# Kernel tuning notes

Measured on AMD Instinct MI355X. Metric: run time of the kernel, lower is better.

The kernel has to match this reference:

```python
import jax, jax.numpy as jnp
import numpy as np

N = 100000      # nodes
E = 1600000     # edges
F_IN = 256      # num_features
H = 128         # hidden_dim
C = 16          # num_classes
LOG_SIGMA0 = float(np.log(0.1))  # prior_sigma = 0.1


def setup_inputs() -> dict:
    key = jax.random.key(0)
    ks = jax.random.split(key, 8)
    x = jax.random.normal(ks[0], (N, F_IN), jnp.float32)
    edge_index = jax.random.randint(ks[1], (2, E), 0, N, dtype=jnp.int64)
    # GCNConv linear weight + bias
    W = jax.random.normal(ks[2], (F_IN, H), jnp.float32) / np.float32(np.sqrt(F_IN))
    gcn_b = jnp.zeros((H,), jnp.float32)
    # BayesLinear params (mu + log_sigma) and fixed sampled noise eps
    w_mu = jax.random.normal(ks[3], (C, H), jnp.float32) / np.float32(np.sqrt(H))
    w_log_sigma = jnp.full((C, H), LOG_SIGMA0, jnp.float32)
    b_mu = jnp.zeros((C,), jnp.float32)
    b_log_sigma = jnp.full((C,), LOG_SIGMA0, jnp.float32)
    eps_w = jax.random.normal(ks[4], (C, H), jnp.float32)
    eps_b = jax.random.normal(ks[5], (C,), jnp.float32)
    return {"x": x, "edge_index": edge_index, "W": W, "gcn_b": gcn_b,
            "w_mu": w_mu, "w_log_sigma": w_log_sigma,
            "b_mu": b_mu, "b_log_sigma": b_log_sigma,
            "eps_w": eps_w, "eps_b": eps_b}


def reference(x, edge_index, W, gcn_b, w_mu, w_log_sigma, b_mu, b_log_sigma, eps_w, eps_b):
    n = x.shape[0]
    # --- GCNConv: add self-loops, symmetric deg^{-1/2} normalization ---
    loop = jnp.arange(n, dtype=edge_index.dtype)
    src = jnp.concatenate([edge_index[0], loop])  # message source j
    dst = jnp.concatenate([edge_index[1], loop])  # aggregation target i
    deg = jax.ops.segment_sum(jnp.ones_like(dst, dtype=x.dtype), dst, num_segments=n)
    deg_inv_sqrt = jnp.where(deg > 0, jax.lax.rsqrt(deg), 0.0)
    norm = deg_inv_sqrt[src] * deg_inv_sqrt[dst]            # [E+N]
    h = x @ W                                               # [N,H] transform first
    msg = h[src] * norm[:, None]                            # [E+N,H] gather
    agg = jax.ops.segment_sum(msg, dst, num_segments=n)     # [N,H] scatter-add
    agg = agg + gcn_b
    # --- ReLU; dropout is identity in eval mode ---
    a = jax.nn.relu(agg)
    # --- BayesLinear: w = mu + exp(log_sigma) * eps ---
    w = w_mu + jnp.exp(w_log_sigma) * eps_w                 # [C,H]
    b = b_mu + jnp.exp(b_log_sigma) * eps_b                 # [C]
    logits = a @ w.T + b                                    # [N,C]
    return jax.nn.log_softmax(logits, axis=1)
```

## Files before the change

kernel.cpp:

```cpp
#include <hip/hip_runtime.h>
#include <hip/hip_bf16.h>

#define N_NODES 100000
#define F_IN    256
#define H_DIM   128
#define C_CLS   16
#define NB_SCAN ((N_NODES + 255) / 256)
#define NSHARD  8
#define SHARD_W ((N_NODES + NSHARD - 1) / NSHARD)
#define ZB      98

typedef __attribute__((ext_vector_type(8))) short  short8;
typedef __attribute__((ext_vector_type(4))) float  float4v;
typedef __attribute__((ext_vector_type(4))) unsigned short ushort4v;

__device__ __forceinline__ float b2f(ushort u) {
    union { unsigned int i; float f; } v;
    v.i = ((unsigned int)u) << 16;
    return v.f;
}

__device__ __forceinline__ ushort f2b(float f) {
    unsigned int x = __float_as_uint(f);
    unsigned int r = (x + 0x7FFFu + ((x >> 16) & 1u)) >> 16;
    return (ushort)r;
}

__device__ __forceinline__ float ldsel(const void* p, int i, int f32f) {
    return f32f ? ((const float*)p)[i] : b2f(((const ushort*)p)[i]);
}

__global__ __launch_bounds__(64) void sniff(const ushort* __restrict__ x,
                                            const int* __restrict__ ei,
                                            int* __restrict__ flags) {
    int lane = threadIdx.x;
    int cnt_bf = 0;
#pragma unroll
    for (int j = 0; j < 4; ++j) {
        ushort u = x[lane * 4 + j];
        int e = (u >> 7) & 0xFF;
        if ((e >= 100 && e <= 140) || (u & 0x7FFF) == 0) cnt_bf++;
    }
    int zodd = (ei[2 * lane + 1] == 0) ? 1 : 0;
#pragma unroll
    for (int off = 32; off >= 1; off >>= 1) {
        cnt_bf += __shfl_xor(cnt_bf, off, 64);
        zodd   += __shfl_xor(zodd,   off, 64);
    }
    if (lane == 0) {
        flags[0] = (cnt_bf < 230) ? 1 : 0;
        flags[1] = (zodd  >= 32) ? 1 : 0;
    }
}

__global__ __launch_bounds__(256) void prep_params(const int* __restrict__ flags,
                                                   const void* __restrict__ W_any,
                                                   ushort* __restrict__ wtg,
                                                   const void* __restrict__ w_mu,
                                                   const void* __restrict__ w_ls,
                                                   const void* __restrict__ eps_w,
                                                   const void* __restrict__ b_mu,
                                                   const void* __restrict__ b_ls,
                                                   const void* __restrict__ eps_b,
                                                   const void* __restrict__ gcn_b,
                                                   ushort* __restrict__ whi,
                                                   ushort* __restrict__ wlo,
                                                   float* __restrict__ bias16,
                                                   float* __restrict__ gcnb_f,
                                                   int* __restrict__ cnt) {
    const int f32f = flags[0];
    const int t = threadIdx.x;
    if (blockIdx.x < H_DIM) {
        const int n = blockIdx.x;
        float v = f32f ? ((const float*)W_any)[t * H_DIM + n]
                       : b2f(((const ushort*)W_any)[t * H_DIM + n]);
        wtg[n * F_IN + t] = f2b(v);
        return;
    }
    if (blockIdx.x > H_DIM) {
        int idx4 = (blockIdx.x - H_DIM - 1) * 256 + t;
        if (idx4 < N_NODES / 4) ((int4*)cnt)[idx4] = make_int4(0, 0, 0, 0);
        return;
    }
#pragma unroll
    for (int i = t; i < C_CLS * H_DIM; i += 256) {
        float v = ldsel(w_mu, i, f32f) + __expf(ldsel(w_ls, i, f32f)) * ldsel(eps_w, i, f32f);
        ushort h = f2b(v);
        whi[i] = h;
        wlo[i] = f2b(v - b2f(h));
    }
    if (t < C_CLS)
        bias16[t] = ldsel(b_mu, t, f32f) + __expf(ldsel(b_ls, t, f32f)) * ldsel(eps_b, t, f32f);
    if (t < H_DIM)
        gcnb_f[t] = ldsel(gcn_b, t, f32f);
}

__global__ __launch_bounds__(256) void prep(const int* __restrict__ flags,
                                            const int* __restrict__ ei,
                                            int* __restrict__ cnt,
                                            int2* __restrict__ pr,
                                            int* __restrict__ rk, int E) {
    int e = blockIdx.x * 256 + threadIdx.x;
    if (e >= E) return;
    int i64 = flags[1];
    int s = i64 ? ei[2L * e]          : ei[e];
    int d = i64 ? ei[2L * E + 2L * e] : ei[(long)E + e];
    pr[e] = make_int2(s, d);
    rk[e] = atomicAdd(&cnt[d], 1);
}

__global__ __launch_bounds__(256) void scan1(const int* __restrict__ cnt,
                                             int* __restrict__ offs,
                                             int* __restrict__ bsum) {
    __shared__ int sd[256];
    int t = threadIdx.x;
    int i = blockIdx.x * 256 + t;
    int v = (i < N_NODES) ? cnt[i] : 0;
    sd[t] = v;
    __syncthreads();
#pragma unroll
    for (int d = 1; d < 256; d <<= 1) {
        int add = (t >= d) ? sd[t - d] : 0;
        __syncthreads();
        sd[t] += add;
        __syncthreads();
    }
    if (i < N_NODES) offs[i] = sd[t] - v;
    if (t == 255) bsum[blockIdx.x] = sd[255];
}

__global__ __launch_bounds__(256) void scan23(int* __restrict__ offs,
                                              const int* __restrict__ bsum,
                                              const int* __restrict__ cnt,
                                              float* __restrict__ dis, int E) {
    __shared__ int ws[4];
    const int t = threadIdx.x;
    const int bid = blockIdx.x;
    const int lane = t & 63;
    const int wave = t >> 6;

    int acc = 0;
    for (int j = t; j < bid; j += 256) acc += bsum[j];
#pragma unroll
    for (int off = 32; off >= 1; off >>= 1) acc += __shfl_xor(acc, off, 64);
    if (lane == 0) ws[wave] = acc;
    __syncthreads();
    const int boffb = ws[0] + ws[1] + ws[2] + ws[3];

    int i = bid * 256 + t;
    if (i == 0) offs[N_NODES] = E;
    if (i >= N_NODES) return;
    offs[i] += boffb;
    dis[i] = rsqrtf((float)(cnt[i] + 1));
}

__global__ __launch_bounds__(256) void build_perm(const int2* __restrict__ pr,
                                                  const int* __restrict__ rk,
                                                  const int* __restrict__ offs,
                                                  int* __restrict__ perm, int E) {
    const int shard = blockIdx.x & (NSHARD - 1);
    const int jb    = blockIdx.x >> 3;
    const int nb    = gridDim.x >> 3;
    const int lo = shard * SHARD_W;
    const int hi = lo + SHARD_W;
    for (int e = jb * 256 + threadIdx.x; e < E; e += nb * 256) {
        int2 p = pr[e];
        if (p.y >= lo && p.y < hi)
            perm[offs[p.y] + rk[e]] = p.x;
    }
}

__global__ __launch_bounds__(256) void gemm_xw(const int* __restrict__ flags,
                                               const void* __restrict__ x_any,
                                               const ushort* __restrict__ wtg,
                                               const float* __restrict__ dis,
                                               ushort* __restrict__ hout) {
    __shared__ __align__(16) ushort wt[128 * 128];
    const int f32f = flags[0];

    const int tid  = threadIdx.x;
    const int lane = tid & 63;
    const int quad = lane >> 4;
    const int lm   = lane & 15;
    const int wave = tid >> 6;

    const int rbase = blockIdx.x * 128 + wave * 32;
    int arow0 = rbase + lm;
    int arow1 = rbase + 16 + lm;
    if (arow0 >= N_NODES) arow0 = N_NODES - 1;
    if (arow1 >= N_NODES) arow1 = N_NODES - 1;
    const float*  xrf0 = (const float*) x_any + (size_t)arow0 * F_IN;
    const float*  xrf1 = (const float*) x_any + (size_t)arow1 * F_IN;
    const ushort* xrb0 = (const ushort*)x_any + (size_t)arow0 * F_IN;
    const ushort* xrb1 = (const ushort*)x_any + (size_t)arow1 * F_IN;

    float4v acc0[8], acc1[8];
#pragma unroll
    for (int c = 0; c < 8; ++c) {
        acc0[c] = (float4v){0.f, 0.f, 0.f, 0.f};
        acc1[c] = (float4v){0.f, 0.f, 0.f, 0.f};
    }

    for (int hh = 0; hh < 2; ++hh) {
        if (hh) __syncthreads();
#pragma unroll
        for (int it = 0; it < 8; ++it) {
            int flat = (it * 256 + tid) * 8;
            int col  = flat >> 7;
            int kloc = flat & 127;
            short8 v = *(const short8*)(wtg + col * F_IN + hh * 128 + kloc);
            int dst = ((col << 7) | kloc) ^ ((col & 7) << 3);
            *(short8*)(wt + dst) = v;
        }
        __syncthreads();
#pragma unroll
        for (int s = 0; s < 4; ++s) {
            int klocal = s * 32 + quad * 8;
            short8 afrag0, afrag1;
            if (f32f) {
                const float* p0 = xrf0 + hh * 128 + klocal;
                const float* p1 = xrf1 + hh * 128 + klocal;
                float4 u0 = *(const float4*)p0;
                float4 u1 = *(const float4*)(p0 + 4);
                float4 u2 = *(const float4*)p1;
                float4 u3 = *(const float4*)(p1 + 4);
                afrag0[0] = (short)f2b(u0.x); afrag0[1] = (short)f2b(u0.y);
                afrag0[2] = (short)f2b(u0.z); afrag0[3] = (short)f2b(u0.w);
                afrag0[4] = (short)f2b(u1.x); afrag0[5] = (short)f2b(u1.y);
                afrag0[6] = (short)f2b(u1.z); afrag0[7] = (short)f2b(u1.w);
                afrag1[0] = (short)f2b(u2.x); afrag1[1] = (short)f2b(u2.y);
                afrag1[2] = (short)f2b(u2.z); afrag1[3] = (short)f2b(u2.w);
                afrag1[4] = (short)f2b(u3.x); afrag1[5] = (short)f2b(u3.y);
                afrag1[6] = (short)f2b(u3.z); afrag1[7] = (short)f2b(u3.w);
            } else {
                afrag0 = *(const short8*)(xrb0 + hh * 128 + klocal);
                afrag1 = *(const short8*)(xrb1 + hh * 128 + klocal);
            }
#pragma unroll
            for (int c = 0; c < 8; ++c) {
                int colr = c * 16 + lm;
                int src = ((colr << 7) | klocal) ^ ((lm & 7) << 3);
                short8 bfrag = *(const short8*)(wt + src);
                acc0[c] = __builtin_amdgcn_mfma_f32_16x16x32_bf16(afrag0, bfrag, acc0[c], 0, 0, 0);
                acc1[c] = __builtin_amdgcn_mfma_f32_16x16x32_bf16(afrag1, bfrag, acc1[c], 0, 0, 0);
            }
        }
    }
    float dv0[4], dv1[4];
#pragma unroll
    for (int r = 0; r < 4; ++r) {
        int n0 = rbase + quad * 4 + r;
        int n1 = rbase + 16 + quad * 4 + r;
        dv0[r] = (n0 < N_NODES) ? dis[n0] : 0.f;
        dv1[r] = (n1 < N_NODES) ? dis[n1] : 0.f;
    }
#pragma unroll
    for (int c = 0; c < 8; ++c) {
        int col = c * 16 + lm;
#pragma unroll
        for (int r = 0; r < 4; ++r) {
            int n0 = rbase + quad * 4 + r;
            int n1 = rbase + 16 + quad * 4 + r;
            if (n0 < N_NODES) hout[(size_t)n0 * H_DIM + col] = f2b(acc0[c][r] * dv0[r]);
            if (n1 < N_NODES) hout[(size_t)n1 * H_DIM + col] = f2b(acc1[c][r] * dv1[r]);
        }
    }
}

__global__ __launch_bounds__(256) void gather_final(const int* __restrict__ flags,
                                                    const int* __restrict__ offs,
                                                    const int* __restrict__ perm,
                                                    const float* __restrict__ dis,
                                                    const ushort* __restrict__ hb,
                                                    const float* __restrict__ gcnb_f,
                                                    const ushort* __restrict__ whi,
                                                    const ushort* __restrict__ wlo,
                                                    const float* __restrict__ bias16,
                                                    void* __restrict__ out) {
    __shared__ __align__(16) ushort alds[16][136];
    const int f32f = flags[0];
    const int lane = threadIdx.x & 63;
    const int wave = threadIdx.x >> 6;
    const int n0 = blockIdx.x * 16;

    for (int r = 0; r < 4; ++r) {
        const int node = n0 + wave * 4 + r;
        const int off0 = __builtin_amdgcn_readfirstlane(offs[node]);
        const int deg  = __builtin_amdgcn_readfirstlane(offs[node + 1]) - off0;
        const int* pp = perm + off0;

        float ax = 0.f, ay = 0.f;
        const int full = deg & ~15;
        for (int base = 0; base < full; base += 16) {
#pragma unroll
            for (int k = 0; k < 16; ++k) {
                int sk = pp[base + k];
                uint u = *((const uint*)(hb + (size_t)sk * H_DIM) + lane);
                ax += __uint_as_float(u << 16);
                ay += __uint_as_float(u & 0xFFFF0000u);
            }
        }
        {
            const int nb = deg - full;
#pragma unroll
            for (int k = 0; k < 16; ++k) {
                int   sk = 0;
                float wk = 0.f;
                if (k < nb) { sk = pp[full + k]; wk = 1.f; }
                uint u = *((const uint*)(hb + (size_t)sk * H_DIM) + lane);
                ax = fmaf(wk, __uint_as_float(u << 16),         ax);
                ay = fmaf(wk, __uint_as_float(u & 0xFFFF0000u), ay);
            }
        }

        const float dd = dis[node];
        uint us = *((const uint*)(hb + (size_t)node * H_DIM) + lane);
        float2 gb = *(const float2*)(gcnb_f + 2 * lane);
        ax = (ax + __uint_as_float(us << 16))         * dd + gb.x;
        ay = (ay + __uint_as_float(us & 0xFFFF0000u)) * dd + gb.y;
        ax = fmaxf(ax, 0.f);
        ay = fmaxf(ay, 0.f);
        uint pack = (uint)f2b(ax) | ((uint)f2b(ay) << 16);
        *((uint*)&alds[wave * 4 + r][2 * lane]) = pack;
    }
    __syncthreads();
    if (wave != 0) return;

    const int lm = lane & 15, quad = lane >> 4;
    const ushort* bh = whi + lm * H_DIM + quad * 8;
    const ushort* bl = wlo + lm * H_DIM + quad * 8;

    float4v acc = (float4v){0.f, 0.f, 0.f, 0.f};
#pragma unroll
    for (int s = 0; s < 4; ++s) {
        short8 af = *(const short8*)&alds[lm][quad * 8 + s * 32];
        short8 b0 = *(const short8*)(bh + s * 32);
        short8 b1 = *(const short8*)(bl + s * 32);
        acc = __builtin_amdgcn_mfma_f32_16x16x32_bf16(af, b0, acc, 0, 0, 0);
        acc = __builtin_amdgcn_mfma_f32_16x16x32_bf16(af, b1, acc, 0, 0, 0);
    }

    const float bias = bias16[lm];
    float p[4], m[4], ss[4];
#pragma unroll
    for (int r = 0; r < 4; ++r) { p[r] = acc[r] + bias; m[r] = p[r]; }
#pragma unroll
    for (int off = 1; off < 16; off <<= 1)
#pragma unroll
        for (int r = 0; r < 4; ++r) m[r] = fmaxf(m[r], __shfl_xor(m[r], off, 64));
#pragma unroll
    for (int r = 0; r < 4; ++r) ss[r] = __expf(p[r] - m[r]);
#pragma unroll
    for (int off = 1; off < 16; off <<= 1)
#pragma unroll
        for (int r = 0; r < 4; ++r) ss[r] += __shfl_xor(ss[r], off, 64);

    if (f32f) {
        float* op = (float*)out;
#pragma unroll
        for (int r = 0; r < 4; ++r)
            op[(size_t)(n0 + quad * 4 + r) * C_CLS + lm] = p[r] - m[r] - __logf(ss[r]);
    } else {
        ushort* op = (ushort*)out;
#pragma unroll
        for (int r = 0; r < 4; ++r)
            op[(size_t)(n0 + quad * 4 + r) * C_CLS + lm] = f2b(p[r] - m[r] - __logf(ss[r]));
    }
}

extern "C" void kernel_launch(void* const* d_in, const int* in_sizes, int n_in,
                              void* d_out, int out_size, void* d_ws, size_t ws_size,
                              hipStream_t stream) {
    const int E = in_sizes[1] / 2;

    char* wp = (char*)d_ws;
    auto alloc = [&](size_t bytes) -> char* {
        char* p = wp; wp += (bytes + 511) & ~(size_t)511; return p;
    };
    int*    flags  = (int*)   alloc(64);
    ushort* hb     = (ushort*)alloc((size_t)N_NODES * H_DIM * 2);
    int*    cnt    = (int*)   alloc((size_t)N_NODES * 4);
    int*    offs   = (int*)   alloc((size_t)(N_NODES + 1) * 4);
    int*    bsum   = (int*)   alloc((size_t)NB_SCAN * 4);
    float*  dis    = (float*) alloc((size_t)N_NODES * 4);
    int*    perm   = (int*)   alloc((size_t)E * 4);
    int2*   pr     = (int2*)  alloc((size_t)E * 8);
    int*    rk     = (int*)   alloc((size_t)E * 4);
    ushort* wtg    = (ushort*)alloc((size_t)H_DIM * F_IN * 2);
    ushort* whi    = (ushort*)alloc((size_t)C_CLS * H_DIM * 2);
    ushort* wlo    = (ushort*)alloc((size_t)C_CLS * H_DIM * 2);
    float*  bias16 = (float*) alloc((size_t)C_CLS * 4);
    float*  gcnb_f = (float*) alloc((size_t)H_DIM * 4);

    sniff<<<1, 64, 0, stream>>>((const ushort*)d_in[0], (const int*)d_in[1], flags);
    prep_params<<<H_DIM + 1 + ZB, 256, 0, stream>>>(flags, d_in[2], wtg,
                                  d_in[4], d_in[5], d_in[8],
                                  d_in[6], d_in[7], d_in[9], d_in[3],
                                  whi, wlo, bias16, gcnb_f, cnt);
    prep<<<(E + 255) / 256, 256, 0, stream>>>(flags, (const int*)d_in[1], cnt, pr, rk, E);
    scan1<<<NB_SCAN, 256, 0, stream>>>(cnt, offs, bsum);
    scan23<<<NB_SCAN, 256, 0, stream>>>(offs, bsum, cnt, dis, E);
    build_perm<<<2048, 256, 0, stream>>>(pr, rk, offs, perm, E);
    gemm_xw<<<(N_NODES + 127) / 128, 256, 0, stream>>>(flags, d_in[0], wtg, dis, hb);
    gather_final<<<N_NODES / 16, 256, 0, stream>>>(flags, offs, perm, dis, hb,
                                                   gcnb_f, whi, wlo, bias16, (void*)d_out);
}
```

Before: 376.2 us.

## Replace CSR build with fixed-width ELL adjacency plus overflow list

Drops the count/scan/permutation pipeline (prep, two scan kernels, build_perm) in favour of one sharded scatter kernel. It writes each edge's source straight into a fixed 64-slot per-node ELL row, with an atomic overflow list for nodes of higher degree. Degree normalisation is now computed inline from the counts, so the separate dis array goes away. This saves several launches and the intermediate pair/rank buffers. The cost is a larger padded ELL array (100k×64 ints) and a linear scan of the overflow list for high-degree nodes.

```diff
diff --git a/kernel.cpp b/kernel.cpp
--- a/kernel.cpp
+++ b/kernel.cpp
@@ -5,9 +5,9 @@
 #define F_IN    256
 #define H_DIM   128
 #define C_CLS   16
-#define NB_SCAN ((N_NODES + 255) / 256)
 #define NSHARD  8
 #define SHARD_W ((N_NODES + NSHARD - 1) / NSHARD)
+#define MAXDEG  64
 #define ZB      98
 
 typedef __attribute__((ext_vector_type(8))) short  short8;
@@ -67,7 +67,8 @@
                                                    ushort* __restrict__ wlo,
                                                    float* __restrict__ bias16,
                                                    float* __restrict__ gcnb_f,
-                                                   int* __restrict__ cnt) {
+                                                   int* __restrict__ cnt,
+                                                   int* __restrict__ ocnt) {
     const int f32f = flags[0];
     const int t = threadIdx.x;
     if (blockIdx.x < H_DIM) {
@@ -82,6 +83,7 @@
         if (idx4 < N_NODES / 4) ((int4*)cnt)[idx4] = make_int4(0, 0, 0, 0);
         return;
     }
+    if (t == 0) *ocnt = 0;
 #pragma unroll
     for (int i = t; i < C_CLS * H_DIM; i += 256) {
         float v = ldsel(w_mu, i, f32f) + __expf(ldsel(w_ls, i, f32f)) * ldsel(eps_w, i, f32f);
@@ -95,85 +97,33 @@
         gcnb_f[t] = ldsel(gcn_b, t, f32f);
 }
 
-__global__ __launch_bounds__(256) void prep(const int* __restrict__ flags,
-                                            const int* __restrict__ ei,
-                                            int* __restrict__ cnt,
-                                            int2* __restrict__ pr,
-                                            int* __restrict__ rk, int E) {
-    int e = blockIdx.x * 256 + threadIdx.x;
-    if (e >= E) return;
-    int i64 = flags[1];
-    int s = i64 ? ei[2L * e]          : ei[e];
-    int d = i64 ? ei[2L * E + 2L * e] : ei[(long)E + e];
-    pr[e] = make_int2(s, d);
-    rk[e] = atomicAdd(&cnt[d], 1);
-}
-
-__global__ __launch_bounds__(256) void scan1(const int* __restrict__ cnt,
-                                             int* __restrict__ offs,
-                                             int* __restrict__ bsum) {
-    __shared__ int sd[256];
-    int t = threadIdx.x;
-    int i = blockIdx.x * 256 + t;
-    int v = (i < N_NODES) ? cnt[i] : 0;
-    sd[t] = v;
-    __syncthreads();
-#pragma unroll
-    for (int d = 1; d < 256; d <<= 1) {
-        int add = (t >= d) ? sd[t - d] : 0;
-        __syncthreads();
-        sd[t] += add;
-        __syncthreads();
-    }
-    if (i < N_NODES) offs[i] = sd[t] - v;
-    if (t == 255) bsum[blockIdx.x] = sd[255];
-}
-
-__global__ __launch_bounds__(256) void scan23(int* __restrict__ offs,
-                                              const int* __restrict__ bsum,
-                                              const int* __restrict__ cnt,
-                                              float* __restrict__ dis, int E) {
-    __shared__ int ws[4];
-    const int t = threadIdx.x;
-    const int bid = blockIdx.x;
-    const int lane = t & 63;
-    const int wave = t >> 6;
-
-    int acc = 0;
-    for (int j = t; j < bid; j += 256) acc += bsum[j];
-#pragma unroll
-    for (int off = 32; off >= 1; off >>= 1) acc += __shfl_xor(acc, off, 64);
-    if (lane == 0) ws[wave] = acc;
-    __syncthreads();
-    const int boffb = ws[0] + ws[1] + ws[2] + ws[3];
-
-    int i = bid * 256 + t;
-    if (i == 0) offs[N_NODES] = E;
-    if (i >= N_NODES) return;
-    offs[i] += boffb;
-    dis[i] = rsqrtf((float)(cnt[i] + 1));
-}
-
-__global__ __launch_bounds__(256) void build_perm(const int2* __restrict__ pr,
-                                                  const int* __restrict__ rk,
-                                                  const int* __restrict__ offs,
-                                                  int* __restrict__ perm, int E) {
+__global__ __launch_bounds__(256) void ell_scatter(const int* __restrict__ flags,
+                                                   const int* __restrict__ ei,
+                                                   int* __restrict__ cnt,
+                                                   int* __restrict__ ell,
+                                                   int2* __restrict__ ovf,
+                                                   int* __restrict__ ocnt, int E) {
     const int shard = blockIdx.x & (NSHARD - 1);
     const int jb    = blockIdx.x >> 3;
     const int nb    = gridDim.x >> 3;
     const int lo = shard * SHARD_W;
     const int hi = lo + SHARD_W;
-    for (int e = jb * 256 + threadIdx.x; e < E; e += nb * 256) {
-        int2 p = pr[e];
-        if (p.y >= lo && p.y < hi)
-            perm[offs[p.y] + rk[e]] = p.x;
+    const int i64 = flags[1];
+    for (long e = (long)jb * 256 + threadIdx.x; e < E; e += (long)nb * 256) {
+        int d = i64 ? ei[2L * E + 2L * e] : ei[(long)E + e];
+        if (d >= lo && d < hi) {
+            int s = i64 ? ei[2L * e] : ei[e];
+            int rk = atomicAdd(&cnt[d], 1);
+            if (rk < MAXDEG) ell[(long)d * MAXDEG + rk] = s;
+            else { int oi = atomicAdd(ocnt, 1); ovf[oi] = make_int2(s, d); }
+        }
     }
 }
 
 __global__ __launch_bounds__(256) void gemm_xw(const int* __restrict__ flags,
                                                const void* __restrict__ x_any,
                                                const ushort* __restrict__ wtg,
-                                               const float* __restrict__ dis,
+                                               const int* __restrict__ cnt,
                                                ushort* __restrict__ hout) {
     __shared__ __align__(16) ushort wt[128 * 128];
     const int f32f = flags[0];
@@ -251,8 +201,8 @@
     for (int r = 0; r < 4; ++r) {
         int n0 = rbase + quad * 4 + r;
         int n1 = rbase + 16 + quad * 4 + r;
-        dv0[r] = (n0 < N_NODES) ? dis[n0] : 0.f;
-        dv1[r] = (n1 < N_NODES) ? dis[n1] : 0.f;
+        dv0[r] = (n0 < N_NODES) ? rsqrtf((float)(cnt[n0] + 1)) : 0.f;
+        dv1[r] = (n1 < N_NODES) ? rsqrtf((float)(cnt[n1] + 1)) : 0.f;
     }
 #pragma unroll
     for (int c = 0; c < 8; ++c) {
@@ -268,9 +218,10 @@
 }
 
 __global__ __launch_bounds__(256) void gather_final(const int* __restrict__ flags,
-                                                    const int* __restrict__ offs,
-                                                    const int* __restrict__ perm,
-                                                    const float* __restrict__ dis,
+                                                    const int* __restrict__ cnt,
+                                                    const int* __restrict__ ell,
+                                                    const int2* __restrict__ ovf,
+                                                    const int* __restrict__ ocnt,
                                                     const ushort* __restrict__ hb,
                                                     const float* __restrict__ gcnb_f,
                                                     const ushort* __restrict__ whi,
@@ -285,9 +236,9 @@
 
     for (int r = 0; r < 4; ++r) {
         const int node = n0 + wave * 4 + r;
-        const int off0 = __builtin_amdgcn_readfirstlane(offs[node]);
-        const int deg  = __builtin_amdgcn_readfirstlane(offs[node + 1]) - off0;
-        const int* pp = perm + off0;
+        const int degt = __builtin_amdgcn_readfirstlane(cnt[node]);
+        const int deg  = degt < MAXDEG ? degt : MAXDEG;
+        const int* pp = ell + (long)node * MAXDEG;
 
         float ax = 0.f, ay = 0.f;
         const int full = deg & ~15;
@@ -312,8 +263,19 @@
                 ay = fmaf(wk, __uint_as_float(u & 0xFFFF0000u), ay);
             }
         }
-
-        const float dd = dis[node];
+        if (degt > MAXDEG) {
+            const int no = __builtin_amdgcn_readfirstlane(*ocnt);
+            for (int j = 0; j < no; ++j) {
+                int2 o = ovf[j];
+                if (o.y == node) {
+                    uint u = *((const uint*)(hb + (size_t)o.x * H_DIM) + lane);
+                    ax += __uint_as_float(u << 16);
+                    ay += __uint_as_float(u & 0xFFFF0000u);
+                }
+            }
+        }
+
+        const float dd = rsqrtf((float)(degt + 1));
         uint us = *((const uint*)(hb + (size_t)node * H_DIM) + lane);
         float2 gb = *(const float2*)(gcnb_f + 2 * lane);
         ax = (ax + __uint_as_float(us << 16))         * dd + gb.x;
@@ -380,12 +342,9 @@
     int*    flags  = (int*)   alloc(64);
     ushort* hb     = (ushort*)alloc((size_t)N_NODES * H_DIM * 2);
     int*    cnt    = (int*)   alloc((size_t)N_NODES * 4);
-    int*    offs   = (int*)   alloc((size_t)(N_NODES + 1) * 4);
-    int*    bsum   = (int*)   alloc((size_t)NB_SCAN * 4);
-    float*  dis    = (float*) alloc((size_t)N_NODES * 4);
-    int*    perm   = (int*)   alloc((size_t)E * 4);
-    int2*   pr     = (int2*)  alloc((size_t)E * 8);
-    int*    rk     = (int*)   alloc((size_t)E * 4);
+    int*    ell    = (int*)   alloc((size_t)N_NODES * MAXDEG * 4);
+    int2*   ovf    = (int2*)  alloc((size_t)E * 8);
+    int*    ocnt   = (int*)   alloc(64);
     ushort* wtg    = (ushort*)alloc((size_t)H_DIM * F_IN * 2);
     ushort* whi    = (ushort*)alloc((size_t)C_CLS * H_DIM * 2);
     ushort* wlo    = (ushort*)alloc((size_t)C_CLS * H_DIM * 2);
@@ -396,12 +355,9 @@
     prep_params<<<H_DIM + 1 + ZB, 256, 0, stream>>>(flags, d_in[2], wtg,
                                   d_in[4], d_in[5], d_in[8],
                                   d_in[6], d_in[7], d_in[9], d_in[3],
-                                  whi, wlo, bias16, gcnb_f, cnt);
-    prep<<<(E + 255) / 256, 256, 0, stream>>>(flags, (const int*)d_in[1], cnt, pr, rk, E);
-    scan1<<<NB_SCAN, 256, 0, stream>>>(cnt, offs, bsum);
-    scan23<<<NB_SCAN, 256, 0, stream>>>(offs, bsum, cnt, dis, E);
-    build_perm<<<2048, 256, 0, stream>>>(pr, rk, offs, perm, E);
-    gemm_xw<<<(N_NODES + 127) / 128, 256, 0, stream>>>(flags, d_in[0], wtg, dis, hb);
-    gather_final<<<N_NODES / 16, 256, 0, stream>>>(flags, offs, perm, dis, hb,
+                                  whi, wlo, bias16, gcnb_f, cnt, ocnt);
+    ell_scatter<<<2048, 256, 0, stream>>>(flags, (const int*)d_in[1], cnt, ell, ovf, ocnt, E);
+    gemm_xw<<<(N_NODES + 127) / 128, 256, 0, stream>>>(flags, d_in[0], wtg, cnt, hb);
+    gather_final<<<N_NODES / 16, 256, 0, stream>>>(flags, cnt, ell, ovf, ocnt, hb,
                                                    gcnb_f, whi, wlo, bias16, (void*)d_out);
 }
```

Measured after the change: 361.8 us. -3.8%, faster.
